# Kernel optimization log

Hardware: AMD Instinct MI355X
Metric: run time of the kernel (lower is better)

The kernel has to match this reference:

```python
import jax, jax.numpy as jnp
import numpy as np

N = 100000
E = 1600000
F_IN = 32   # node_features
F_H = 32    # filters
F_OUT = 4


def setup_inputs() -> dict:
    key = jax.random.key(0)
    ks = jax.random.split(key, 24)
    inp = {
        'x': jax.random.normal(ks[0], (N, F_IN), dtype=jnp.float32),
        'edge_index': jax.random.randint(ks[1], (2, E), 0, N, dtype=jnp.int64),
        'edge_weight': jax.random.uniform(ks[2], (E,), dtype=jnp.float32),
        'H': jax.random.normal(ks[3], (N, F_H), dtype=jnp.float32),
    }
    # ChebConv params: W[k] for k in {0,1} (K=2), bias per conv.
    def cheb_params(kw, kb, fin):
        s = 1.0 / np.sqrt(fin)
        W = jax.random.uniform(kw, (2, fin, F_H), jnp.float32, -s, s)
        b = jax.random.uniform(kb, (F_H,), jnp.float32, -s, s)
        return W, b
    names = ['xz', 'hz', 'xr', 'hr', 'xh', 'hh']
    fins = [F_IN, F_H, F_IN, F_H, F_IN, F_H]
    for i, (nm, fin) in enumerate(zip(names, fins)):
        W, b = cheb_params(ks[4 + 2 * i], ks[5 + 2 * i], fin)
        inp['W' + nm] = W
        inp['b' + nm] = b
    s = 1.0 / np.sqrt(F_H)
    inp['lin_w'] = jax.random.uniform(ks[20], (F_H, F_OUT), jnp.float32, -s, s)
    inp['lin_b'] = jax.random.uniform(ks[21], (F_OUT,), jnp.float32, -s, s)
    return inp


def _cheb(x, src, dst, nw, W, b):
    # ChebConv, K=2, sym norm, lambda_max=2 => L_hat = -D^{-1/2} A D^{-1/2}
    # (diagonal of scaled Laplacian cancels exactly: 1 - 1 = 0).
    tx1 = -jax.ops.segment_sum(nw[:, None] * x[src], dst, num_segments=N)
    return x @ W[0] + tx1 @ W[1] + b


def reference(x, edge_index, edge_weight, H,
              Wxz, bxz, Whz, bhz, Wxr, bxr, Whr, bhr, Wxh, bxh, Whh, bhh,
              lin_w, lin_b):
    src, dst = edge_index[0], edge_index[1]
    # remove_self_loops equivalent: zero out self-loop weights
    w = jnp.where(src == dst, 0.0, edge_weight)
    deg = jax.ops.segment_sum(w, src, num_segments=N)
    dinv = jnp.where(deg > 0, jax.lax.rsqrt(jnp.maximum(deg, 1e-30)), 0.0)
    nw = dinv[src] * w * dinv[dst]  # per-edge sym-normalized weight

    Z = jax.nn.sigmoid(_cheb(x, src, dst, nw, Wxz, bxz) +
                       _cheb(H, src, dst, nw, Whz, bhz))
    R = jax.nn.sigmoid(_cheb(x, src, dst, nw, Wxr, bxr) +
                       _cheb(H, src, dst, nw, Whr, bhr))
    H_tilde = jnp.tanh(_cheb(x, src, dst, nw, Wxh, bxh) +
                       _cheb(H * R, src, dst, nw, Whh, bhh))
    h = Z * H + (1.0 - Z) * H_tilde
    out = jax.nn.relu(h) @ lin_w + lin_b
    return (out, h)
```

## Files before the change

kernel.cpp:

```cpp
#include <hip/hip_runtime.h>
#include <hip/hip_bf16.h>
#include <hip/hip_fp16.h>

typedef __hip_bfloat16 bf16;
typedef __attribute__((ext_vector_type(8))) short bf16x8;
typedef __attribute__((ext_vector_type(4))) float f32x4;

#define NN   100000
#define EE   1600000
#define FH   32
#define FOUT 4
#define NBD  782
#define NBS  196
#define CAPB 2432
#define CAPS 8960
#define CAP  64
#define BINBLK 512
#define BINTHR 1024
#define EPB  3125
#define EPT  4
#define MFMA16(a, b, c) __builtin_amdgcn_mfma_f32_16x16x32_bf16(a, b, c, 0, 0, 0)

__device__ __forceinline__ float b2f(bf16 v) { return __bfloat162float(v); }

__device__ __forceinline__ float ldf(const void* p, int i, int f32) {
    return f32 ? ((const float*)p)[i] : b2f(((const bf16*)p)[i]);
}
__device__ __forceinline__ int ldi(const void* p, int i, int i64f) {
    return i64f ? (int)(((const long long*)p)[i]) : ((const int*)p)[i];
}
__device__ __forceinline__ void stf(void* p, int i, int f32, float v) {
    if (f32) ((float*)p)[i] = v;
    else     ((bf16*)p)[i] = __float2bfloat16(v);
}
__device__ __forceinline__ float h2f(unsigned short u) {
    return __half2float(__ushort_as_half(u));
}
__device__ __forceinline__ unsigned short f2h16(float v) {
    return __half_as_ushort(__float2half(v));
}
__device__ __forceinline__ short f2bf(float v) {
    unsigned u = __float_as_uint(v);
    return (short)((u + 0x7FFFu + ((u >> 16) & 1u)) >> 16);
}
__device__ __forceinline__ unsigned q8(float v) {
    int q = (int)rintf(v * 16.f) + 128;
    q = q < 0 ? 0 : (q > 255 ? 255 : q);
    return (unsigned)q;
}
__device__ __forceinline__ float ub(unsigned w, int k) {
    return (float)((w >> (k * 8)) & 0xFFu);
}
__device__ __forceinline__ float4 bfly_g(float4 v) {
    v.x += __shfl_xor(v.x, 8);  v.y += __shfl_xor(v.y, 8);
    v.z += __shfl_xor(v.z, 8);  v.w += __shfl_xor(v.w, 8);
    v.x += __shfl_xor(v.x, 16); v.y += __shfl_xor(v.y, 16);
    v.z += __shfl_xor(v.z, 16); v.w += __shfl_xor(v.w, 16);
    return v;
}
__device__ __forceinline__ bf16x8 bfragT(const short* __restrict__ wt, int idx) {
    return *(const bf16x8*)(wt + idx);
}

__global__ __launch_bounds__(256) void k_prep(
    const void* __restrict__ x, const void* __restrict__ H,
    const void* __restrict__ ei,
    const void* __restrict__ W0, const void* __restrict__ W1,
    const void* __restrict__ W2, const void* __restrict__ W3,
    const void* __restrict__ W4, const void* __restrict__ W5,
    int* __restrict__ flg, int* __restrict__ binCur, int* __restrict__ binCurS,
    short* __restrict__ wt, unsigned* __restrict__ xh,
    unsigned short* __restrict__ xh8) {
    __shared__ int s_fl[2];
    int t = threadIdx.x, b = blockIdx.x;
    if (t == 0) { s_fl[0] = 0; s_fl[1] = 0; }
    __syncthreads();
    {
        float v = b2f(((const bf16*)x)[t]);
        if ((!isfinite(v)) || (fabsf(v) > 100.f)) atomicOr(&s_fl[0], 1);
        int w32 = ((const int*)ei)[t];
        if ((t & 1) && (w32 != 0)) atomicOr(&s_fl[1], 1);
    }
    __syncthreads();
    int f32 = s_fl[0];
    int i64 = s_fl[1] ? 0 : 1;
    if (b == 0 && t == 0) { flg[0] = f32; flg[1] = i64; }
    if (b < 48) {
        int i = b * 256 + t;
        int mat = i >> 11;
        int r = i & 2047;
        int cheb = r >> 10, k = (r >> 5) & 31, n = r & 31;
        const void* W = (mat == 0) ? W0 : (mat == 1) ? W1 : (mat == 2) ? W2
                      : (mat == 3) ? W3 : (mat == 4) ? W4 : W5;
        wt[(((mat << 1) + cheb) << 10) + n * 32 + k] = f2bf(ldf(W, r, f32));
    } else if (b == 48) {
        for (int i = t; i < NBD; i += 256) binCur[i] = i * CAPB;
    } else if (b == 49) {
        for (int i = t; i < NBS; i += 256) binCurS[i] = i * CAPS;
    }
    int i = b * 256 + t;
    if (i < NN * FH) {
        float xv = ldf(x, i, f32);
        float hv = ldf(H, i, f32);
        xh[i] = ((unsigned)f2h16(hv) << 16) | f2h16(xv);
        xh8[i] = (unsigned short)((q8(hv) << 8) | q8(xv));
    }
}

__global__ __launch_bounds__(BINTHR, 8) void k_bin(const void* __restrict__ ei,
                                                   const void* __restrict__ ew,
                                                   const int* __restrict__ flg,
                                                   int* __restrict__ binCur,
                                                   int* __restrict__ binCurS,
                                                   int* __restrict__ dstRecA,
                                                   unsigned char* __restrict__ dstRecB,
                                                   int* __restrict__ srcRec) {
    __shared__ int hD[NBD], bD[NBD], lofD[NBD];
    __shared__ int hS[NBS], bS[NBS], lofS[NBS];
    __shared__ int sWave[16];
    __shared__ int2 stD[EPB];
    __shared__ int  stS[EPB];
    int t = threadIdx.x;
    int lane = t & 63, wv = t >> 6;
    for (int i = t; i < NBD; i += BINTHR) hD[i] = 0;
    for (int i = t; i < NBS; i += BINTHR) hS[i] = 0;
    __syncthreads();
    int e0 = blockIdx.x * EPB;
    int e1 = e0 + EPB;
    int f32 = flg[0], i64 = flg[1];
    int rs[EPT], rd[EPT], rw[EPT];
    #pragma unroll
    for (int u = 0; u < EPT; u++) {
        int e = e0 + t + u * BINTHR;
        bool v = e < e1;
        int s = v ? ldi(ei, e, i64) : 0;
        int d = v ? ldi(ei, EE + e, i64) : 0;
        float w = (v && s != d) ? ldf(ew, e, f32) : 0.f;
        rs[u] = s; rd[u] = d;
        rw[u] = (int)(f2h16(w) & 0x7FFFu);
        if (v) {
            atomicAdd(&hD[d >> 7], 1);
            atomicAdd(&hS[s >> 9], 1);
        }
    }
    __syncthreads();
    for (int i = t; i < NBD; i += BINTHR)
        bD[i] = (hD[i] > 0) ? atomicAdd(&binCur[i], hD[i]) : 0;
    for (int i = t; i < NBS; i += BINTHR)
        bS[i] = (hS[i] > 0) ? atomicAdd(&binCurS[i], hS[i]) : 0;
    int vD = (t < NBD) ? hD[t] : 0;
    int p = vD;
    #pragma unroll
    for (int ofs = 1; ofs < 64; ofs <<= 1) {
        int u = __shfl_up(p, ofs);
        if (lane >= ofs) p += u;
    }
    if (lane == 63) sWave[wv] = p;
    __syncthreads();
    if (t < 16) {
        int q = sWave[t];
        #pragma unroll
        for (int ofs = 1; ofs < 16; ofs <<= 1) {
            int u = __shfl_up(q, ofs);
            if (t >= ofs) q += u;
        }
        sWave[t] = q;
    }
    __syncthreads();
    if (t < NBD) {
        int incl = p + (wv ? sWave[wv - 1] : 0);
        lofD[t] = incl - vD;
        hD[t] = 0;
    }
    __syncthreads();
    int vS = (t < NBS) ? hS[t] : 0;
    p = vS;
    #pragma unroll
    for (int ofs = 1; ofs < 64; ofs <<= 1) {
        int u = __shfl_up(p, ofs);
        if (lane >= ofs) p += u;
    }
    if (lane == 63) sWave[wv] = p;
    __syncthreads();
    if (t < 16) {
        int q = sWave[t];
        #pragma unroll
        for (int ofs = 1; ofs < 16; ofs <<= 1) {
            int u = __shfl_up(q, ofs);
            if (t >= ofs) q += u;
        }
        sWave[t] = q;
    }
    __syncthreads();
    if (t < NBS) {
        int incl = p + (wv ? sWave[wv - 1] : 0);
        lofS[t] = incl - vS;
        hS[t] = 0;
    }
    __syncthreads();
    #pragma unroll
    for (int u = 0; u < EPT; u++) {
        int e = e0 + t + u * BINTHR;
        if (e < e1) {
            int s = rs[u], d = rd[u], wh = rw[u];
            int bd = d >> 7, bs = s >> 9;
            int rdx = atomicAdd(&hD[bd], 1);
            int rsx = atomicAdd(&hS[bs], 1);
            stD[lofD[bd] + rdx] = make_int2((int)(((unsigned)s << 15) | wh),
                                            (bd << 8) | (d & 127));
            stS[lofS[bs] + rsx] = (int)(((unsigned)bs << 24) |
                                        ((unsigned)(s & 511) << 15) | (unsigned)wh);
        }
    }
    __syncthreads();
    int tot = e1 - e0;
    for (int i = t; i < tot; i += BINTHR) {
        int2 r = stD[i];
        int bin = ((unsigned)r.y) >> 8;
        int g = bD[bin] + (i - lofD[bin]);
        if (g < (bin + 1) * CAPB) {
            dstRecA[g] = r.x;
            dstRecB[g] = (unsigned char)(r.y & 127);
        }
        int u = stS[i];
        int sbin = ((unsigned)u) >> 24;
        int gs = bS[sbin] + (i - lofS[sbin]);
        if (gs < (sbin + 1) * CAPS) srcRec[gs] = u & 0xFFFFFF;
    }
}

__global__ __launch_bounds__(256) void k_degb(const int* __restrict__ binCurS,
                                              const int* __restrict__ srcRec,
                                              float* __restrict__ dinv) {
    __shared__ float lDeg[512];
    int b = blockIdx.x, t = threadIdx.x;
    lDeg[t] = 0.f; lDeg[t + 256] = 0.f;
    __syncthreads();
    int cnt = binCurS[b] - b * CAPS;
    if (cnt > CAPS) cnt = CAPS;
    for (int i = t; i < cnt; i += 256) {
        int r = srcRec[b * CAPS + i];
        atomicAdd(&lDeg[(r >> 15) & 511], h2f((unsigned short)(r & 0x7FFF)));
    }
    __syncthreads();
    #pragma unroll
    for (int k = 0; k < 2; k++) {
        int li = t + k * 256;
        int node = b * 512 + li;
        if (node < NN) {
            float dv = lDeg[li];
            dinv[node] = (dv > 0.f) ? rsqrtf(dv) : 0.f;
        }
    }
}

__global__ __launch_bounds__(256) void k_fillb(const int* __restrict__ binCur,
                                               const int* __restrict__ dstRecA,
                                               const unsigned char* __restrict__ dstRecB,
                                               const float* __restrict__ dinv,
                                               int* __restrict__ cursor,
                                               int* __restrict__ ell) {
    __shared__ int lCur[128];
    __shared__ int lEll[128 * CAP];
    int b = blockIdx.x, t = threadIdx.x;
    if (t < 128) lCur[t] = 0;
    __syncthreads();
    int cnt = binCur[b] - b * CAPB;
    if (cnt > CAPB) cnt = CAPB;
    for (int i = t; i < cnt; i += 256) {
        int ra = dstRecA[b * CAPB + i];
        int d7 = dstRecB[b * CAPB + i];
        int slot = atomicAdd(&lCur[d7], 1);
        if (slot < CAP) {
            unsigned s = ((unsigned)ra) >> 15;
            float c = dinv[s] * h2f((unsigned short)(ra & 0x7FFF));
            lEll[d7 * CAP + slot] = (int)((s << 15) | (f2h16(c) & 0x7FFFu));
        }
    }
    __syncthreads();
    int nodeBase = b * 128;
    for (int i = t; i < 128 * CAP; i += 256) {
        int node = nodeBase + (i >> 6);
        if (node < NN && (i & 63) < lCur[i >> 6])
            ell[(size_t)node * CAP + (i & (CAP - 1))] = lEll[i];
    }
    if (t < 128 && nodeBase + t < NN) {
        int c = lCur[t]; if (c > CAP) c = CAP;
        cursor[nodeBase + t] = c;
    }
}

__global__ __launch_bounds__(256, 8) void k_gather1(const int* __restrict__ cursor,
                                                    const int* __restrict__ ell,
                                                    const float* __restrict__ dinv,
                                                    const unsigned short* __restrict__ xh8,
                                                    unsigned* __restrict__ axah) {
    int t = threadIdx.x;
    int node = blockIdx.x * 8 + (t >> 5);
    if (node >= NN) return;
    int f = t & 31;
    int g = f >> 3, c = f & 7;
    int cnt = cursor[node];
    size_t base = (size_t)node * CAP;
    float4 ax = {0.f, 0.f, 0.f, 0.f}, ah = {0.f, 0.f, 0.f, 0.f};
    float cs = 0.f;
    for (int j = 0; j < cnt; j += 16) {
        int wrd[4]; float cf[4]; uint2 pv[4];
        #pragma unroll
        for (int u = 0; u < 4; u++) {
            int jj = j + u * 4 + g;
            wrd[u] = (jj < cnt) ? ell[base + jj] : 0;
        }
        #pragma unroll
        for (int u = 0; u < 4; u++) {
            int s = ((unsigned)wrd[u]) >> 15;
            cf[u] = h2f((unsigned short)(wrd[u] & 0x7FFF));
            pv[u] = ((const uint2*)xh8)[s * 8 + c];
        }
        #pragma unroll
        for (int u = 0; u < 4; u++) {
            cs += cf[u];
            ax.x += cf[u] * ub(pv[u].x, 0);
            ah.x += cf[u] * ub(pv[u].x, 1);
            ax.y += cf[u] * ub(pv[u].x, 2);
            ah.y += cf[u] * ub(pv[u].x, 3);
            ax.z += cf[u] * ub(pv[u].y, 0);
            ah.z += cf[u] * ub(pv[u].y, 1);
            ax.w += cf[u] * ub(pv[u].y, 2);
            ah.w += cf[u] * ub(pv[u].y, 3);
        }
    }
    ax = bfly_g(ax); ah = bfly_g(ah);
    cs += __shfl_xor(cs, 8);
    cs += __shfl_xor(cs, 16);
    if (g == 0) {
        float dd = -dinv[node];
        float bias = 8.f * cs;
        uint4 o;
        o.x = ((unsigned)f2h16(dd * (ah.x * 0.0625f - bias)) << 16)
            | f2h16(dd * (ax.x * 0.0625f - bias));
        o.y = ((unsigned)f2h16(dd * (ah.y * 0.0625f - bias)) << 16)
            | f2h16(dd * (ax.y * 0.0625f - bias));
        o.z = ((unsigned)f2h16(dd * (ah.z * 0.0625f - bias)) << 16)
            | f2h16(dd * (ax.z * 0.0625f - bias));
        o.w = ((unsigned)f2h16(dd * (ah.w * 0.0625f - bias)) << 16)
            | f2h16(dd * (ax.w * 0.0625f - bias));
        ((uint4*)(axah + (size_t)node * FH))[c] = o;
    }
}

__global__ __launch_bounds__(256) void k_r_mfma(
    const unsigned* __restrict__ xh, const unsigned* __restrict__ axah,
    const int* __restrict__ flg, const short* __restrict__ wt,
    const void* __restrict__ bxr, const void* __restrict__ bhr,
    unsigned short* __restrict__ hr16) {
    int t = threadIdx.x;
    int lane = t & 63, wv = t >> 6;
    int f32 = flg[0];
    int c = lane & 15, quad = lane >> 4, kb = quad * 8;
    int nodeBase = blockIdx.x * 64 + wv * 16;
    int nm = nodeBase + c; if (nm >= NN) nm = NN - 1;

    bf16x8 fx, fHH, fAX, fAH;
    {
        const uint4* p = (const uint4*)(xh + (size_t)nm * FH + kb);
        uint4 a = p[0], b = p[1];
        unsigned wd[8] = {a.x, a.y, a.z, a.w, b.x, b.y, b.z, b.w};
        #pragma unroll
        for (int j = 0; j < 8; j++) {
            fx[j]  = f2bf(h2f((unsigned short)(wd[j] & 0xFFFF)));
            fHH[j] = f2bf(h2f((unsigned short)(wd[j] >> 16)));
        }
    }
    {
        const uint4* p = (const uint4*)(axah + (size_t)nm * FH + kb);
        uint4 a = p[0], b = p[1];
        unsigned wd[8] = {a.x, a.y, a.z, a.w, b.x, b.y, b.z, b.w};
        #pragma unroll
        for (int j = 0; j < 8; j++) {
            fAX[j] = f2bf(h2f((unsigned short)(wd[j] & 0xFFFF)));
            fAH[j] = f2bf(h2f((unsigned short)(wd[j] >> 16)));
        }
    }

    float br0 = ldf(bxr, c, f32) + ldf(bhr, c, f32);
    float br1 = ldf(bxr, c + 16, f32) + ldf(bhr, c + 16, f32);
    f32x4 ar0 = {br0, br0, br0, br0}, ar1 = {br1, br1, br1, br1};

    int i0 = c * 32 + kb;
    int i1 = (c + 16) * 32 + kb;
    ar0 = MFMA16(fx,  bfragT(wt, 4 * 1024 + i0), ar0);
    ar0 = MFMA16(fAX, bfragT(wt, 5 * 1024 + i0), ar0);
    ar0 = MFMA16(fHH, bfragT(wt, 6 * 1024 + i0), ar0);
    ar0 = MFMA16(fAH, bfragT(wt, 7 * 1024 + i0), ar0);
    ar1 = MFMA16(fx,  bfragT(wt, 4 * 1024 + i1), ar1);
    ar1 = MFMA16(fAX, bfragT(wt, 5 * 1024 + i1), ar1);
    ar1 = MFMA16(fHH, bfragT(wt, 6 * 1024 + i1), ar1);
    ar1 = MFMA16(fAH, bfragT(wt, 7 * 1024 + i1), ar1);

    #pragma unroll
    for (int tl = 0; tl < 2; tl++) {
        f32x4 ar = tl ? ar1 : ar0;
        int f = c + 16 * tl;
        #pragma unroll
        for (int r = 0; r < 4; r++) {
            int node = nodeBase + quad * 4 + r;
            if (node < NN) {
                float rv = 1.f / (1.f + expf(-ar[r]));
                float Hv = h2f((unsigned short)(xh[(size_t)node * FH + f] >> 16));
                hr16[(size_t)node * FH + f] = f2h16(Hv * rv);
            }
        }
    }
}

__global__ __launch_bounds__(256, 8) void k_gather2(const int* __restrict__ cursor,
                                                    const int* __restrict__ ell,
                                                    const float* __restrict__ dinv,
                                                    const unsigned short* __restrict__ hr16,
                                                    unsigned short* __restrict__ ahr16) {
    int t = threadIdx.x;
    int node = blockIdx.x * 8 + (t >> 5);
    if (node >= NN) return;
    int f = t & 31;
    int g = f >> 3, c = f & 7;
    int cnt = cursor[node];
    size_t base = (size_t)node * CAP;
    float4 acc = {0.f, 0.f, 0.f, 0.f};
    for (int j = 0; j < cnt; j += 16) {
        int wrd[4]; float cf[4]; ushort4 hv[4];
        #pragma unroll
        for (int u = 0; u < 4; u++) {
            int jj = j + u * 4 + g;
            wrd[u] = (jj < cnt) ? ell[base + jj] : 0;
        }
        #pragma unroll
        for (int u = 0; u < 4; u++) {
            int s = ((unsigned)wrd[u]) >> 15;
            cf[u] = h2f((unsigned short)(wrd[u] & 0x7FFF));
            hv[u] = ((const ushort4*)hr16)[s * 8 + c];
        }
        #pragma unroll
        for (int u = 0; u < 4; u++) {
            acc.x += cf[u] * h2f(hv[u].x);
            acc.y += cf[u] * h2f(hv[u].y);
            acc.z += cf[u] * h2f(hv[u].z);
            acc.w += cf[u] * h2f(hv[u].w);
        }
    }
    acc = bfly_g(acc);
    if (g == 0) {
        float dd = -dinv[node];
        ushort4 o = {f2h16(dd * acc.x), f2h16(dd * acc.y),
                     f2h16(dd * acc.z), f2h16(dd * acc.w)};
        ((ushort4*)(ahr16 + (size_t)node * FH))[c] = o;
    }
}

__global__ __launch_bounds__(256) void k_final(
    const unsigned* __restrict__ xh, const unsigned* __restrict__ axah,
    const int* __restrict__ flg, const short* __restrict__ wt,
    const unsigned short* __restrict__ hr16,
    const unsigned short* __restrict__ ahr16,
    const void* __restrict__ bxz, const void* __restrict__ bhz,
    const void* __restrict__ bxh, const void* __restrict__ bhh,
    const void* __restrict__ lin_w, const void* __restrict__ lin_b,
    void* __restrict__ out) {
    __shared__ float srh[64][FH + 1];
    __shared__ float slw[FH * FOUT];
    __shared__ float slb[FOUT];

    int t = threadIdx.x;
    int lane = t & 63, wv = t >> 6;
    int f32 = flg[0];
    int c = lane & 15, quad = lane >> 4, kb = quad * 8;
    int nodeBase = blockIdx.x * 64 + wv * 16;
    int nm = nodeBase + c; if (nm >= NN) nm = NN - 1;

    if (t < FH * FOUT) slw[t] = ldf(lin_w, t, f32);
    if (t < FOUT) slb[t] = ldf(lin_b, t, f32);

    bf16x8 fx, fHH, fAX, fAH, fHR, fAHR;
    {
        const uint4* p = (const uint4*)(xh + (size_t)nm * FH + kb);
        uint4 a = p[0], b = p[1];
        unsigned wd[8] = {a.x, a.y, a.z, a.w, b.x, b.y, b.z, b.w};
        #pragma unroll
        for (int j = 0; j < 8; j++) {
            fx[j]  = f2bf(h2f((unsigned short)(wd[j] & 0xFFFF)));
            fHH[j] = f2bf(h2f((unsigned short)(wd[j] >> 16)));
        }
    }
    {
        const uint4* p = (const uint4*)(axah + (size_t)nm * FH + kb);
        uint4 a = p[0], b = p[1];
        unsigned wd[8] = {a.x, a.y, a.z, a.w, b.x, b.y, b.z, b.w};
        #pragma unroll
        for (int j = 0; j < 8; j++) {
            fAX[j] = f2bf(h2f((unsigned short)(wd[j] & 0xFFFF)));
            fAH[j] = f2bf(h2f((unsigned short)(wd[j] >> 16)));
        }
    }
    {
        const uint4* p = (const uint4*)(hr16 + (size_t)nm * FH + kb);
        uint4 a = p[0];
        unsigned wd[4] = {a.x, a.y, a.z, a.w};
        #pragma unroll
        for (int j = 0; j < 8; j++)
            fHR[j] = f2bf(h2f((unsigned short)((wd[j >> 1] >> ((j & 1) * 16)) & 0xFFFF)));
    }
    {
        const uint4* p = (const uint4*)(ahr16 + (size_t)nm * FH + kb);
        uint4 a = p[0];
        unsigned wd[4] = {a.x, a.y, a.z, a.w};
        #pragma unroll
        for (int j = 0; j < 8; j++)
            fAHR[j] = f2bf(h2f((unsigned short)((wd[j >> 1] >> ((j & 1) * 16)) & 0xFFFF)));
    }

    float bz0 = ldf(bxz, c, f32) + ldf(bhz, c, f32);
    float bz1 = ldf(bxz, c + 16, f32) + ldf(bhz, c + 16, f32);
    float bh0 = ldf(bxh, c, f32) + ldf(bhh, c, f32);
    float bh1 = ldf(bxh, c + 16, f32) + ldf(bhh, c + 16, f32);
    f32x4 az0 = {bz0, bz0, bz0, bz0}, az1 = {bz1, bz1, bz1, bz1};
    f32x4 a0 = {bh0, bh0, bh0, bh0}, a1 = {bh1, bh1, bh1, bh1};

    int i0 = c * 32 + kb;
    int i1 = (c + 16) * 32 + kb;
    az0 = MFMA16(fx,   bfragT(wt,  0 * 1024 + i0), az0);
    az0 = MFMA16(fAX,  bfragT(wt,  1 * 1024 + i0), az0);
    az0 = MFMA16(fHH,  bfragT(wt,  2 * 1024 + i0), az0);
    az0 = MFMA16(fAH,  bfragT(wt,  3 * 1024 + i0), az0);
    az1 = MFMA16(fx,   bfragT(wt,  0 * 1024 + i1), az1);
    az1 = MFMA16(fAX,  bfragT(wt,  1 * 1024 + i1), az1);
    az1 = MFMA16(fHH,  bfragT(wt,  2 * 1024 + i1), az1);
    az1 = MFMA16(fAH,  bfragT(wt,  3 * 1024 + i1), az1);
    a0 = MFMA16(fx,   bfragT(wt,  8 * 1024 + i0), a0);
    a0 = MFMA16(fAX,  bfragT(wt,  9 * 1024 + i0), a0);
    a0 = MFMA16(fHR,  bfragT(wt, 10 * 1024 + i0), a0);
    a0 = MFMA16(fAHR, bfragT(wt, 11 * 1024 + i0), a0);
    a1 = MFMA16(fx,   bfragT(wt,  8 * 1024 + i1), a1);
    a1 = MFMA16(fAX,  bfragT(wt,  9 * 1024 + i1), a1);
    a1 = MFMA16(fHR,  bfragT(wt, 10 * 1024 + i1), a1);
    a1 = MFMA16(fAHR, bfragT(wt, 11 * 1024 + i1), a1);

    #pragma unroll
    for (int tl = 0; tl < 2; tl++) {
        f32x4 a = tl ? a1 : a0;
        f32x4 az = tl ? az1 : az0;
        int f = c + 16 * tl;
        #pragma unroll
        for (int r = 0; r < 4; r++) {
            int node = nodeBase + quad * 4 + r;
            if (node < NN) {
                float ht = tanhf(a[r]);
                float zv = 1.f / (1.f + expf(-az[r]));
                float Hv = h2f((unsigned short)(xh[(size_t)node * FH + f] >> 16));
                float hval = zv * Hv + (1.f - zv) * ht;
                stf(out, NN * FOUT + node * FH + f, f32, hval);
                srh[wv * 16 + quad * 4 + r][f] = hval > 0.f ? hval : 0.f;
            }
        }
    }
    __syncthreads();

    int nl = t >> 2, fo = t & 3;
    int node2 = blockIdx.x * 64 + nl;
    if (node2 < NN) {
        float acc = slb[fo];
        #pragma unroll
        for (int k = 0; k < FH; k++) acc += srh[nl][k] * slw[k * FOUT + fo];
        stf(out, node2 * FOUT + fo, f32, acc);
    }
}

extern "C" void kernel_launch(void* const* d_in, const int* in_sizes, int n_in,
                              void* d_out, int out_size, void* d_ws, size_t ws_size,
                              hipStream_t stream) {
    const void* x   = d_in[0];
    const void* ei  = d_in[1];
    const void* ew  = d_in[2];
    const void* H   = d_in[3];
    const void* Wxz = d_in[4];
    const void* bxz = d_in[5];
    const void* Whz = d_in[6];
    const void* bhz = d_in[7];
    const void* Wxr = d_in[8];
    const void* bxr = d_in[9];
    const void* Whr = d_in[10];
    const void* bhr = d_in[11];
    const void* Wxh = d_in[12];
    const void* bxh = d_in[13];
    const void* Whh = d_in[14];
    const void* bhh = d_in[15];
    const void* lnw = d_in[16];
    const void* lnb = d_in[17];

    char* base = (char*)d_ws;
    int*            flg     = (int*)base;            base += 64;
    int*            binCur  = (int*)base;            base += (NBD * 4 + 63) & ~63;
    int*            binCurS = (int*)base;            base += (NBS * 4 + 63) & ~63;
    float*          dinv    = (float*)base;          base += (size_t)NN * 4;
    int*            cursor  = (int*)base;            base += (size_t)NN * 4;
    short*          wt      = (short*)base;          base += (12288 * 2 + 63) & ~63;
    unsigned*       xh      = (unsigned*)base;       base += (size_t)NN * FH * 4;
    unsigned short* xh8     = (unsigned short*)base; base += (size_t)NN * FH * 2;
    unsigned*       axah    = (unsigned*)base;       base += (size_t)NN * FH * 4;
    unsigned short* hr16    = (unsigned short*)base; base += (size_t)NN * FH * 2;
    unsigned short* ahr16   = (unsigned short*)base; base += (size_t)NN * FH * 2;
    int*            ell     = (int*)base;            base += (size_t)NN * CAP * 4;
    int*            dstRecA = (int*)base;            base += (size_t)NBD * CAPB * 4;
    unsigned char*  dstRecB = (unsigned char*)base;  base += ((size_t)NBD * CAPB + 63) & ~(size_t)63;
    int*            srcRec  = (int*)base;

    const int pb   = (NN * FH + 255) / 256;
    const int n8b  = (NN + 7) / 8;
    const int n64b = (NN + 63) / 64;

    k_prep<<<pb, 256, 0, stream>>>(x, H, ei, Wxz, Whz, Wxr, Whr, Wxh, Whh,
                                   flg, binCur, binCurS, wt, xh, xh8);
    k_bin<<<BINBLK, BINTHR, 0, stream>>>(ei, ew, flg, binCur, binCurS,
                                         dstRecA, dstRecB, srcRec);
    k_degb<<<NBS, 256, 0, stream>>>(binCurS, srcRec, dinv);
    k_fillb<<<NBD, 256, 0, stream>>>(binCur, dstRecA, dstRecB, dinv,
                                     cursor, ell);
    k_gather1<<<n8b, 256, 0, stream>>>(cursor, ell, dinv, xh8, axah);
    k_r_mfma<<<n64b, 256, 0, stream>>>(xh, axah, flg, wt, bxr, bhr, hr16);
    k_gather2<<<n8b, 256, 0, stream>>>(cursor, ell, dinv, hr16, ahr16);
    k_final<<<n64b, 256, 0, stream>>>(xh, axah, flg, wt, hr16, ahr16,
                                      bxz, bhz, bxh, bhh, lnw, lnb, d_out);
}
```

Measured before the change: 259.2 us.

## Fuse prep and edge binning into one launch with memset-initialized bin cursors

Merges the input-conversion kernel and the edge-binning kernel into a single launch, with the first blocks doing binning and the remaining blocks converting x/H and weights. Bin cursors are now zeroed by a memset and offset by bin base inside the kernel, which removes the dependency on the prep kernel having initialized them. This removes one launch and lets the conversion overlap with binning. In exchange, prep blocks now carry the large shared-memory footprint of the binning blocks, which limits occupancy. The launch-bounds occupancy hints on the gather kernels are also dropped.

```diff
diff --git a/kernel.cpp b/kernel.cpp
--- a/kernel.cpp
+++ b/kernel.cpp
@@ -19,6 +19,7 @@
 #define BINTHR 1024
 #define EPB  3125
 #define EPT  4
+#define PREPB 3125
 #define MFMA16(a, b, c) __builtin_amdgcn_mfma_f32_16x16x32_bf16(a, b, c, 0, 0, 0)
 
 __device__ __forceinline__ float b2f(bf16 v) { return __bfloat162float(v); }
@@ -62,20 +63,28 @@
     return *(const bf16x8*)(wt + idx);
 }
 
-__global__ __launch_bounds__(256) void k_prep(
+__global__ __launch_bounds__(BINTHR, 8) void k_pb(
     const void* __restrict__ x, const void* __restrict__ H,
-    const void* __restrict__ ei,
+    const void* __restrict__ ei, const void* __restrict__ ew,
     const void* __restrict__ W0, const void* __restrict__ W1,
     const void* __restrict__ W2, const void* __restrict__ W3,
     const void* __restrict__ W4, const void* __restrict__ W5,
     int* __restrict__ flg, int* __restrict__ binCur, int* __restrict__ binCurS,
     short* __restrict__ wt, unsigned* __restrict__ xh,
-    unsigned short* __restrict__ xh8) {
+    unsigned short* __restrict__ xh8,
+    int* __restrict__ dstRecA, unsigned char* __restrict__ dstRecB,
+    int* __restrict__ srcRec) {
+    __shared__ int hD[NBD], bD[NBD], lofD[NBD];
+    __shared__ int hS[NBS], bS[NBS], lofS[NBS];
+    __shared__ int sWave[16];
     __shared__ int s_fl[2];
+    __shared__ int2 stD[EPB];
+    __shared__ int  stS[EPB];
     int t = threadIdx.x, b = blockIdx.x;
+    int lane = t & 63, wv = t >> 6;
     if (t == 0) { s_fl[0] = 0; s_fl[1] = 0; }
     __syncthreads();
-    {
+    if (t < 256) {
         float v = b2f(((const bf16*)x)[t]);
         if ((!isfinite(v)) || (fabsf(v) > 100.f)) atomicOr(&s_fl[0], 1);
         int w32 = ((const int*)ei)[t];
@@ -85,49 +94,29 @@
     int f32 = s_fl[0];
     int i64 = s_fl[1] ? 0 : 1;
     if (b == 0 && t == 0) { flg[0] = f32; flg[1] = i64; }
-    if (b < 48) {
-        int i = b * 256 + t;
-        int mat = i >> 11;
-        int r = i & 2047;
-        int cheb = r >> 10, k = (r >> 5) & 31, n = r & 31;
-        const void* W = (mat == 0) ? W0 : (mat == 1) ? W1 : (mat == 2) ? W2
-                      : (mat == 3) ? W3 : (mat == 4) ? W4 : W5;
-        wt[(((mat << 1) + cheb) << 10) + n * 32 + k] = f2bf(ldf(W, r, f32));
-    } else if (b == 48) {
-        for (int i = t; i < NBD; i += 256) binCur[i] = i * CAPB;
-    } else if (b == 49) {
-        for (int i = t; i < NBS; i += 256) binCurS[i] = i * CAPS;
-    }
-    int i = b * 256 + t;
-    if (i < NN * FH) {
+
+    if (b >= BINBLK) {
+        int i = (b - BINBLK) * BINTHR + t;
+        if (i < 12288) {
+            int mat = i >> 11;
+            int r = i & 2047;
+            int cheb = r >> 10, k = (r >> 5) & 31, n = r & 31;
+            const void* W = (mat == 0) ? W0 : (mat == 1) ? W1 : (mat == 2) ? W2
+                          : (mat == 3) ? W3 : (mat == 4) ? W4 : W5;
+            wt[(((mat << 1) + cheb) << 10) + n * 32 + k] = f2bf(ldf(W, r, f32));
+        }
         float xv = ldf(x, i, f32);
         float hv = ldf(H, i, f32);
         xh[i] = ((unsigned)f2h16(hv) << 16) | f2h16(xv);
         xh8[i] = (unsigned short)((q8(hv) << 8) | q8(xv));
-    }
-}
-
-__global__ __launch_bounds__(BINTHR, 8) void k_bin(const void* __restrict__ ei,
-                                                   const void* __restrict__ ew,
-                                                   const int* __restrict__ flg,
-                                                   int* __restrict__ binCur,
-                                                   int* __restrict__ binCurS,
-                                                   int* __restrict__ dstRecA,
-                                                   unsigned char* __restrict__ dstRecB,
-                                                   int* __restrict__ srcRec) {
-    __shared__ int hD[NBD], bD[NBD], lofD[NBD];
-    __shared__ int hS[NBS], bS[NBS], lofS[NBS];
-    __shared__ int sWave[16];
-    __shared__ int2 stD[EPB];
-    __shared__ int  stS[EPB];
-    int t = threadIdx.x;
-    int lane = t & 63, wv = t >> 6;
+        return;
+    }
+
     for (int i = t; i < NBD; i += BINTHR) hD[i] = 0;
     for (int i = t; i < NBS; i += BINTHR) hS[i] = 0;
     __syncthreads();
-    int e0 = blockIdx.x * EPB;
+    int e0 = b * EPB;
     int e1 = e0 + EPB;
-    int f32 = flg[0], i64 = flg[1];
     int rs[EPT], rd[EPT], rw[EPT];
     #pragma unroll
     for (int u = 0; u < EPT; u++) {
@@ -145,9 +134,9 @@
     }
     __syncthreads();
     for (int i = t; i < NBD; i += BINTHR)
-        bD[i] = (hD[i] > 0) ? atomicAdd(&binCur[i], hD[i]) : 0;
+        bD[i] = i * CAPB + ((hD[i] > 0) ? atomicAdd(&binCur[i], hD[i]) : 0);
     for (int i = t; i < NBS; i += BINTHR)
-        bS[i] = (hS[i] > 0) ? atomicAdd(&binCurS[i], hS[i]) : 0;
+        bS[i] = i * CAPS + ((hS[i] > 0) ? atomicAdd(&binCurS[i], hS[i]) : 0);
     int vD = (t < NBD) ? hD[t] : 0;
     int p = vD;
     #pragma unroll
@@ -236,7 +225,7 @@
     int b = blockIdx.x, t = threadIdx.x;
     lDeg[t] = 0.f; lDeg[t + 256] = 0.f;
     __syncthreads();
-    int cnt = binCurS[b] - b * CAPS;
+    int cnt = binCurS[b];
     if (cnt > CAPS) cnt = CAPS;
     for (int i = t; i < cnt; i += 256) {
         int r = srcRec[b * CAPS + i];
@@ -265,7 +254,7 @@
     int b = blockIdx.x, t = threadIdx.x;
     if (t < 128) lCur[t] = 0;
     __syncthreads();
-    int cnt = binCur[b] - b * CAPB;
+    int cnt = binCur[b];
     if (cnt > CAPB) cnt = CAPB;
     for (int i = t; i < cnt; i += 256) {
         int ra = dstRecA[b * CAPB + i];
@@ -290,11 +279,11 @@
     }
 }
 
-__global__ __launch_bounds__(256, 8) void k_gather1(const int* __restrict__ cursor,
-                                                    const int* __restrict__ ell,
-                                                    const float* __restrict__ dinv,
-                                                    const unsigned short* __restrict__ xh8,
-                                                    unsigned* __restrict__ axah) {
+__global__ __launch_bounds__(256) void k_gather1(const int* __restrict__ cursor,
+                                                 const int* __restrict__ ell,
+                                                 const float* __restrict__ dinv,
+                                                 const unsigned short* __restrict__ xh8,
+                                                 unsigned* __restrict__ axah) {
     int t = threadIdx.x;
     int node = blockIdx.x * 8 + (t >> 5);
     if (node >= NN) return;
@@ -414,11 +403,11 @@
     }
 }
 
-__global__ __launch_bounds__(256, 8) void k_gather2(const int* __restrict__ cursor,
-                                                    const int* __restrict__ ell,
-                                                    const float* __restrict__ dinv,
-                                                    const unsigned short* __restrict__ hr16,
-                                                    unsigned short* __restrict__ ahr16) {
+__global__ __launch_bounds__(256) void k_gather2(const int* __restrict__ cursor,
+                                                 const int* __restrict__ ell,
+                                                 const float* __restrict__ dinv,
+                                                 const unsigned short* __restrict__ hr16,
+                                                 unsigned short* __restrict__ ahr16) {
     int t = threadIdx.x;
     int node = blockIdx.x * 8 + (t >> 5);
     if (node >= NN) return;
@@ -597,9 +586,11 @@
     const void* lnb = d_in[17];
 
     char* base = (char*)d_ws;
+    size_t binCurBytes  = (NBD * 4 + 63) & ~63;
+    size_t binCurSBytes = (NBS * 4 + 63) & ~63;
     int*            flg     = (int*)base;            base += 64;
-    int*            binCur  = (int*)base;            base += (NBD * 4 + 63) & ~63;
-    int*            binCurS = (int*)base;            base += (NBS * 4 + 63) & ~63;
+    int*            binCur  = (int*)base;            base += binCurBytes;
+    int*            binCurS = (int*)base;            base += binCurSBytes;
     float*          dinv    = (float*)base;          base += (size_t)NN * 4;
     int*            cursor  = (int*)base;            base += (size_t)NN * 4;
     short*          wt      = (short*)base;          base += (12288 * 2 + 63) & ~63;
@@ -613,14 +604,15 @@
     unsigned char*  dstRecB = (unsigned char*)base;  base += ((size_t)NBD * CAPB + 63) & ~(size_t)63;
     int*            srcRec  = (int*)base;
 
-    const int pb   = (NN * FH + 255) / 256;
     const int n8b  = (NN + 7) / 8;
     const int n64b = (NN + 63) / 64;
 
-    k_prep<<<pb, 256, 0, stream>>>(x, H, ei, Wxz, Whz, Wxr, Whr, Wxh, Whh,
-                                   flg, binCur, binCurS, wt, xh, xh8);
-    k_bin<<<BINBLK, BINTHR, 0, stream>>>(ei, ew, flg, binCur, binCurS,
-                                         dstRecA, dstRecB, srcRec);
+    hipMemsetAsync(binCur, 0, binCurBytes + binCurSBytes, stream);
+    k_pb<<<BINBLK + PREPB, BINTHR, 0, stream>>>(x, H, ei, ew,
+                                                Wxz, Whz, Wxr, Whr, Wxh, Whh,
+                                                flg, binCur, binCurS, wt,
+                                                xh, xh8,
+                                                dstRecA, dstRecB, srcRec);
     k_degb<<<NBS, 256, 0, stream>>>(binCurS, srcRec, dinv);
     k_fillb<<<NBD, 256, 0, stream>>>(binCur, dstRecA, dstRecB, dinv,
                                      cursor, ell);
```

Result: no change. 262.9 us (+1.4%).
